# Performance work log

Hardware: AMD Instinct MI355X
Metric: run time of the kernel (lower is better)

The kernel has to match this reference:

```python
import jax, jax.numpy as jnp
import numpy as np

B, N, L = 16, 512, 2048          # batch, decoder word positions, lstm char positions
DIM, M, CE, VOCAB, H = 768, 8, 64, 1024, 128  # hidden, max_word_len, char_emb, vocab, lstm hidden


def setup_inputs() -> dict:
    key = jax.random.key(0)
    ks = jax.random.split(key, 10)
    return {
        "dec_hidden": jax.random.normal(ks[0], (B, N, DIM), jnp.float32),
        "lstm_input_ids": jax.random.randint(ks[1], (B, L), 0, VOCAB),
        "lstm_word_lens": jax.random.randint(ks[2], (B, N), 0, M + 1),
        "char_emb": jax.random.normal(ks[3], (VOCAB, CE), jnp.float32) * 0.02,
        "W_proj": jax.random.normal(ks[4], (DIM, CE * M), jnp.float32) * 0.02,
        "b_proj": jnp.zeros((CE * M,), jnp.float32),
        "W_ih": jax.random.normal(ks[5], (4 * H, 2 * CE), jnp.float32) * 0.05,
        "W_hh": jax.random.normal(ks[6], (4 * H, H), jnp.float32) * 0.05,
        "b_ih": jnp.zeros((4 * H,), jnp.float32),
        "b_hh": jnp.zeros((4 * H,), jnp.float32),
        "W_pred": jax.random.normal(ks[7], (H, VOCAB), jnp.float32) * 0.02,
        "b_pred": jnp.zeros((VOCAB,), jnp.float32),
    }


def _gather_pad(rep, lens):
    """Ragged select + left-compact + zero-pad for one batch element.
    rep: [N, M, CE] per-word char projections; lens: [N] word lengths in [0, M].
    Equivalent to: rep[mask] (ragged), truncated to L, written into zeros[L, CE]."""
    mask = jnp.arange(M) < lens[:, None]                 # [N, M]
    mflat = mask.reshape(-1)                             # [N*M]
    dest = jnp.cumsum(mflat) - 1                         # compacted destination index
    # invalid or overflowing entries are dumped into a scratch row L (dropped)
    dest = jnp.where(mflat & (dest < L), dest, L)
    vals = rep.reshape(-1, CE) * mflat[:, None].astype(rep.dtype)
    buf = jnp.zeros((L + 1, CE), rep.dtype).at[dest].set(vals)
    return buf[:L]


def _lstm(x, W_ih, W_hh, b_ih, b_hh):
    """PyTorch-convention single-layer LSTM. x: [B, T, in]. Gates order i,f,g,o."""
    def step(carry, xt):
        h, c = carry
        g = xt @ W_ih.T + b_ih + h @ W_hh.T + b_hh       # [B, 4H]
        i, f, gg, o = jnp.split(g, 4, axis=-1)
        c = jax.nn.sigmoid(f) * c + jax.nn.sigmoid(i) * jnp.tanh(gg)
        h = jax.nn.sigmoid(o) * jnp.tanh(c)
        return (h, c), h
    h0 = jnp.zeros((x.shape[0], H), x.dtype)
    _, hs = jax.lax.scan(step, (h0, h0), jnp.swapaxes(x, 0, 1))
    return jnp.swapaxes(hs, 0, 1)                        # [B, T, H]


def reference(dec_hidden, lstm_input_ids, lstm_word_lens, char_emb, W_proj, b_proj,
              W_ih, W_hh, b_ih, b_hh, W_pred, b_pred):
    dec_char = char_emb[lstm_input_ids]                  # [B, L, CE]
    # hidden_proj: b n (m d) -> b n m d
    rep = (dec_hidden @ W_proj + b_proj).reshape(B, N, M, CE)
    padded = jax.vmap(_gather_pad)(rep, lstm_word_lens)  # [B, L, CE]
    x = jnp.concatenate([dec_char, padded], axis=-1)     # [B, L, 2*CE]
    hs = _lstm(x, W_ih, W_hh, b_ih, b_hh)                # [B, L, H]
    return hs @ W_pred + b_pred                          # [B, L, VOCAB]
```

## Files before the change

### kernel.cpp

```cpp
#include <hip/hip_runtime.h>
#include <cstdint>
#include <cstddef>

#define B_    16
#define N_    512
#define L_    2048
#define DIM_  768
#define M_    8
#define CE_   64
#define VOCAB_ 1024
#define H_    128
#define G4_   512
#define XDIM_ 128

typedef __bf16 bf16x8 __attribute__((ext_vector_type(8)));
typedef float  f32x4  __attribute__((ext_vector_type(4)));

__device__ __forceinline__ unsigned short f2bf(float f) {
    unsigned u = __float_as_uint(f);
    u += 0x7fffu + ((u >> 16) & 1u);
    return (unsigned short)(u >> 16);
}

template<bool TRANSB>
__global__ __launch_bounds__(256) void gemm_f32(
    const float* __restrict__ A, const float* __restrict__ Bm,
    const float* __restrict__ bias1, const float* __restrict__ bias2,
    float* __restrict__ C, int M, int N, int K)
{
    __shared__ float As[2][8][128];
    __shared__ float Bs[2][8][128];
    const int t  = threadIdx.x;
    const int tx = t & 15, ty = t >> 4;
    const int m0 = blockIdx.y * 128, n0 = blockIdx.x * 128;
    const int arow = t >> 1, ahalf = (t & 1) * 4;
    const int bk = t >> 5, bn = (t & 31) * 4;

    float acc[8][8];
#pragma unroll
    for (int i = 0; i < 8; i++)
#pragma unroll
        for (int j = 0; j < 8; j++) acc[i][j] = 0.f;

    {
        float4 av = *(const float4*)(A + (size_t)(m0 + arow) * K + ahalf);
        float4 bv;
        if (TRANSB) bv = *(const float4*)(Bm + (size_t)(n0 + arow) * K + ahalf);
        else        bv = *(const float4*)(Bm + (size_t)bk * N + n0 + bn);
        As[0][ahalf + 0][arow] = av.x;
        As[0][ahalf + 1][arow] = av.y;
        As[0][ahalf + 2][arow] = av.z;
        As[0][ahalf + 3][arow] = av.w;
        if (TRANSB) {
            Bs[0][ahalf + 0][arow] = bv.x;
            Bs[0][ahalf + 1][arow] = bv.y;
            Bs[0][ahalf + 2][arow] = bv.z;
            Bs[0][ahalf + 3][arow] = bv.w;
        } else {
            *(float4*)&Bs[0][bk][bn] = bv;
        }
    }
    __syncthreads();

    int cur = 0;
    for (int k0 = 0; k0 < K; k0 += 8) {
        const bool more = (k0 + 8 < K);
        float4 av, bv;
        if (more) {
            av = *(const float4*)(A + (size_t)(m0 + arow) * K + (k0 + 8) + ahalf);
            if (TRANSB) bv = *(const float4*)(Bm + (size_t)(n0 + arow) * K + (k0 + 8) + ahalf);
            else        bv = *(const float4*)(Bm + (size_t)(k0 + 8 + bk) * N + n0 + bn);
        }
#pragma unroll
        for (int k = 0; k < 8; k++) {
            float a[8], bb[8];
            *(float4*)&a[0]  = *(const float4*)&As[cur][k][ty * 8];
            *(float4*)&a[4]  = *(const float4*)&As[cur][k][ty * 8 + 4];
            *(float4*)&bb[0] = *(const float4*)&Bs[cur][k][tx * 8];
            *(float4*)&bb[4] = *(const float4*)&Bs[cur][k][tx * 8 + 4];
#pragma unroll
            for (int i = 0; i < 8; i++)
#pragma unroll
                for (int j = 0; j < 8; j++)
                    acc[i][j] = fmaf(a[i], bb[j], acc[i][j]);
        }
        if (more) {
            const int nxt = cur ^ 1;
            As[nxt][ahalf + 0][arow] = av.x;
            As[nxt][ahalf + 1][arow] = av.y;
            As[nxt][ahalf + 2][arow] = av.z;
            As[nxt][ahalf + 3][arow] = av.w;
            if (TRANSB) {
                Bs[nxt][ahalf + 0][arow] = bv.x;
                Bs[nxt][ahalf + 1][arow] = bv.y;
                Bs[nxt][ahalf + 2][arow] = bv.z;
                Bs[nxt][ahalf + 3][arow] = bv.w;
            } else {
                *(float4*)&Bs[nxt][bk][bn] = bv;
            }
        }
        __syncthreads();
        cur ^= 1;
    }

    float bia[8];
#pragma unroll
    for (int j = 0; j < 8; j++) {
        int gn = n0 + tx * 8 + j;
        bia[j] = bias1[gn] + (bias2 ? bias2[gn] : 0.f);
    }
#pragma unroll
    for (int i = 0; i < 8; i++) {
        size_t row = (size_t)(m0 + ty * 8 + i) * N + n0 + tx * 8;
#pragma unroll
        for (int j = 0; j < 8; j++)
            C[row + j] = acc[i][j] + bia[j];
    }
}

__global__ __launch_bounds__(512) void scan_lens(const int* __restrict__ lens,
                                                 int* __restrict__ off)
{
    const int b = blockIdx.x, t = threadIdx.x;
    __shared__ int s[512];
    int v = lens[b * N_ + t];
    s[t] = v;
    __syncthreads();
    for (int d = 1; d < 512; d <<= 1) {
        int u = (t >= d) ? s[t - d] : 0;
        __syncthreads();
        s[t] += u;
        __syncthreads();
    }
    off[b * N_ + t] = s[t] - v;
}

__global__ __launch_bounds__(256) void char_gather(const int* __restrict__ ids,
                                                   const float* __restrict__ emb,
                                                   float* __restrict__ x)
{
    int g   = blockIdx.x * 8 + (threadIdx.x >> 5);
    int l32 = threadIdx.x & 31;
    int id  = ids[g];
    float4 v;
    if (l32 < 16) v = *(const float4*)(emb + (size_t)id * CE_ + l32 * 4);
    else          v = make_float4(0.f, 0.f, 0.f, 0.f);
    *(float4*)(x + (size_t)g * XDIM_ + l32 * 4) = v;
}

__global__ __launch_bounds__(512) void scatter_pad(const float* __restrict__ rep,
                                                   const int* __restrict__ lens,
                                                   const int* __restrict__ off,
                                                   float* __restrict__ x)
{
    int word = blockIdx.x;
    int b = word >> 9;
    int m  = threadIdx.x >> 6;
    int cc = threadIdx.x & 63;
    int len = lens[word];
    if (m < len) {
        int dst = off[word] + m;
        if (dst < L_) {
            x[((size_t)b * L_ + dst) * XDIM_ + CE_ + cc] =
                rep[((size_t)word * M_ + m) * CE_ + cc];
        }
    }
}

__global__ __launch_bounds__(512) void lstm_rec(const float* __restrict__ gx,
                                                const float* __restrict__ Whh,
                                                float* __restrict__ hs)
{
    const int b    = blockIdx.x;
    const int tid  = threadIdx.x;
    const int wave = tid >> 6, lane = tid & 63;
    const int quad = lane >> 4, l15 = lane & 15;
    const int j    = wave * 16 + l15;

    __shared__ __align__(16) unsigned short hbuf[2][128];
    if (tid < 128) hbuf[0][tid] = 0;

    bf16x8 bfrag[4][4];
#pragma unroll
    for (int q = 0; q < 4; q++) {
        const float* wrow = Whh + (size_t)(q * 128 + j) * H_;
#pragma unroll
        for (int kk = 0; kk < 4; kk++) {
            int kb = kk * 32 + quad * 8;
            float4 w0 = *(const float4*)(wrow + kb);
            float4 w1 = *(const float4*)(wrow + kb + 4);
            union { unsigned short u[8]; bf16x8 v; } U;
            U.u[0] = f2bf(w0.x); U.u[1] = f2bf(w0.y); U.u[2] = f2bf(w0.z); U.u[3] = f2bf(w0.w);
            U.u[4] = f2bf(w1.x); U.u[5] = f2bf(w1.y); U.u[6] = f2bf(w1.z); U.u[7] = f2bf(w1.w);
            bfrag[q][kk] = U.v;
        }
    }

    const float* gxb = gx + (size_t)b * L_ * G4_ + j;
    float pf[4][4];
#pragma unroll
    for (int u = 0; u < 4; u++)
#pragma unroll
        for (int q = 0; q < 4; q++)
            pf[u][q] = gxb[(size_t)u * G4_ + q * 128];

    float c = 0.f;
    float* hsb = hs + (size_t)b * L_ * H_;
    __syncthreads();

#define RCP_(x) __builtin_amdgcn_rcpf(x)
#define MFMA_(a, bb, cc) __builtin_amdgcn_mfma_f32_16x16x32_bf16(a, bb, cc, 0, 0, 0)

    for (int t0 = 0; t0 < L_; t0 += 4) {
#pragma unroll
        for (int u = 0; u < 4; u++) {
            const int t  = t0 + u;
            const int pb = t & 1;

            bf16x8 a0 = *(const bf16x8*)&hbuf[pb][0 * 32 + quad * 8];
            bf16x8 a1 = *(const bf16x8*)&hbuf[pb][1 * 32 + quad * 8];
            bf16x8 a2 = *(const bf16x8*)&hbuf[pb][2 * 32 + quad * 8];
            bf16x8 a3 = *(const bf16x8*)&hbuf[pb][3 * 32 + quad * 8];

            f32x4 accga = {pf[u][2], 0.f, 0.f, 0.f};
            f32x4 accgb = {0.f, 0.f, 0.f, 0.f};
            f32x4 acci  = {pf[u][0], 0.f, 0.f, 0.f};
            f32x4 accf  = {pf[u][1], 0.f, 0.f, 0.f};
            f32x4 acco  = {pf[u][3], 0.f, 0.f, 0.f};

            {
                int tn = t + 4; if (tn > L_ - 1) tn = L_ - 1;
#pragma unroll
                for (int q = 0; q < 4; q++) pf[u][q] = gxb[(size_t)tn * G4_ + q * 128];
            }

            accga = MFMA_(a0, bfrag[2][0], accga);
            accgb = MFMA_(a1, bfrag[2][1], accgb);
            acci  = MFMA_(a0, bfrag[0][0], acci);
            accf  = MFMA_(a0, bfrag[1][0], accf);
            acco  = MFMA_(a0, bfrag[3][0], acco);
            accga = MFMA_(a2, bfrag[2][2], accga);
            accgb = MFMA_(a3, bfrag[2][3], accgb);
            acci  = MFMA_(a1, bfrag[0][1], acci);
            accf  = MFMA_(a1, bfrag[1][1], accf);
            acco  = MFMA_(a1, bfrag[3][1], acco);
            acci  = MFMA_(a2, bfrag[0][2], acci);
            accf  = MFMA_(a2, bfrag[1][2], accf);
            acco  = MFMA_(a2, bfrag[3][2], acco);
            acci  = MFMA_(a3, bfrag[0][3], acci);
            accf  = MFMA_(a3, bfrag[1][3], accf);
            acco  = MFMA_(a3, bfrag[3][3], acco);

            float gg = accga[0] + accgb[0];
            float tg = 1.f - 2.f * RCP_(__expf(2.f * gg) + 1.f);
            float si = RCP_(1.f + __expf(-acci[0]));
            float sf = RCP_(1.f + __expf(-accf[0]));
            float so = RCP_(1.f + __expf(-acco[0]));
            c = sf * c + si * tg;
            float tc = 1.f - 2.f * RCP_(__expf(2.f * c) + 1.f);
            float h = so * tc;

            unsigned hr;
            asm("v_cvt_pk_bf16_f32 %0, %1, %2" : "=v"(hr) : "v"(h), "v"(h));
            if (quad == 0) {
                hbuf[pb ^ 1][j] = (unsigned short)hr;
                hsb[(size_t)t * H_ + j] = h;
            }
            asm volatile("s_waitcnt lgkmcnt(0)\n\ts_barrier" ::: "memory");
        }
    }
#undef RCP_
#undef MFMA_
}

extern "C" void kernel_launch(void* const* d_in, const int* in_sizes, int n_in,
                              void* d_out, int out_size, void* d_ws, size_t ws_size,
                              hipStream_t stream)
{
    (void)in_sizes; (void)n_in; (void)out_size; (void)ws_size;
    const float* dec_hidden = (const float*)d_in[0];
    const int*   ids        = (const int*)d_in[1];
    const int*   lens       = (const int*)d_in[2];
    const float* char_emb   = (const float*)d_in[3];
    const float* W_proj     = (const float*)d_in[4];
    const float* b_proj     = (const float*)d_in[5];
    const float* W_ih       = (const float*)d_in[6];
    const float* W_hh       = (const float*)d_in[7];
    const float* b_ih       = (const float*)d_in[8];
    const float* b_hh       = (const float*)d_in[9];
    const float* W_pred     = (const float*)d_in[10];
    const float* b_pred     = (const float*)d_in[11];
    float* out = (float*)d_out;

    char* ws   = (char*)d_ws;
    float* rep = (float*)(ws);
    float* x   = (float*)(ws + (size_t)16 * 1024 * 1024);
    float* hs  = (float*)(ws + (size_t)32 * 1024 * 1024);
    int*   off = (int*)  (ws + (size_t)48 * 1024 * 1024);
    float* gx  = out;

    gemm_f32<false><<<dim3(4, 64), 256, 0, stream>>>(
        dec_hidden, W_proj, b_proj, nullptr, rep, B_ * N_, 512, DIM_);

    scan_lens<<<B_, 512, 0, stream>>>(lens, off);

    char_gather<<<(B_ * L_) / 8, 256, 0, stream>>>(ids, char_emb, x);
    scatter_pad<<<B_ * N_, 512, 0, stream>>>(rep, lens, off, x);

    gemm_f32<true><<<dim3(4, 256), 256, 0, stream>>>(
        x, W_ih, b_ih, b_hh, gx, B_ * L_, G4_, XDIM_);

    lstm_rec<<<B_, 512, 0, stream>>>(gx, W_hh, hs);

    gemm_f32<false><<<dim3(8, 256), 256, 0, stream>>>(
        hs, W_pred, b_pred, nullptr, out, B_ * L_, VOCAB_, H_);
}
```

Measured before the change: 1.366 ms.

## Halve LSTM recurrence block to 4 waves, each computing two hidden-unit groups

```diff
diff --git a/kernel.cpp b/kernel.cpp
--- a/kernel.cpp
+++ b/kernel.cpp
@@ -167,53 +167,64 @@
     }
 }
 
-__global__ __launch_bounds__(512) void lstm_rec(const float* __restrict__ gx,
-                                                const float* __restrict__ Whh,
-                                                float* __restrict__ hs)
+__global__ __launch_bounds__(256, 1) void lstm_rec(const float* __restrict__ gx,
+                                                   const float* __restrict__ Whh,
+                                                   float* __restrict__ hs)
 {
     const int b    = blockIdx.x;
     const int tid  = threadIdx.x;
     const int wave = tid >> 6, lane = tid & 63;
     const int quad = lane >> 4, l15 = lane & 15;
-    const int j    = wave * 16 + l15;
+    const int jA   = wave * 32 + l15;
 
     __shared__ __align__(16) unsigned short hbuf[2][128];
     if (tid < 128) hbuf[0][tid] = 0;
 
-    bf16x8 bfrag[4][4];
-#pragma unroll
-    for (int q = 0; q < 4; q++) {
-        const float* wrow = Whh + (size_t)(q * 128 + j) * H_;
-#pragma unroll
-        for (int kk = 0; kk < 4; kk++) {
-            int kb = kk * 32 + quad * 8;
-            float4 w0 = *(const float4*)(wrow + kb);
-            float4 w1 = *(const float4*)(wrow + kb + 4);
-            union { unsigned short u[8]; bf16x8 v; } U;
-            U.u[0] = f2bf(w0.x); U.u[1] = f2bf(w0.y); U.u[2] = f2bf(w0.z); U.u[3] = f2bf(w0.w);
-            U.u[4] = f2bf(w1.x); U.u[5] = f2bf(w1.y); U.u[6] = f2bf(w1.z); U.u[7] = f2bf(w1.w);
-            bfrag[q][kk] = U.v;
-        }
-    }
-
-    const float* gxb = gx + (size_t)b * L_ * G4_ + j;
-    float pf[4][4];
-#pragma unroll
-    for (int u = 0; u < 4; u++)
-#pragma unroll
-        for (int q = 0; q < 4; q++)
-            pf[u][q] = gxb[(size_t)u * G4_ + q * 128];
+    bf16x8 bfrag[2][4][4];
+#pragma unroll
+    for (int jg = 0; jg < 2; jg++)
+#pragma unroll
+        for (int q = 0; q < 4; q++) {
+            const float* wrow = Whh + (size_t)(q * 128 + jA + jg * 16) * H_;
+#pragma unroll
+            for (int kk = 0; kk < 4; kk++) {
+                int kb = kk * 32 + quad * 8;
+                float4 w0 = *(const float4*)(wrow + kb);
+                float4 w1 = *(const float4*)(wrow + kb + 4);
+                union { unsigned short u[8]; bf16x8 v; } U;
+                U.u[0] = f2bf(w0.x); U.u[1] = f2bf(w0.y); U.u[2] = f2bf(w0.z); U.u[3] = f2bf(w0.w);
+                U.u[4] = f2bf(w1.x); U.u[5] = f2bf(w1.y); U.u[6] = f2bf(w1.z); U.u[7] = f2bf(w1.w);
+                bfrag[jg][q][kk] = U.v;
+            }
+        }
+
+    const float* gp = gx + (size_t)b * L_ * G4_ + jA;
+    float pf[2][2][4];
+#pragma unroll
+    for (int u = 0; u < 2; u++)
+#pragma unroll
+        for (int jg = 0; jg < 2; jg++)
+#pragma unroll
+            for (int q = 0; q < 4; q++)
+                pf[u][jg][q] = gp[(size_t)u * G4_ + q * 128 + jg * 16];
+    gp += 2 * G4_;
+
+    f32x4 aAi = {0,0,0,0}, aAf = aAi, aAg = aAi, aAo = aAi;
+    f32x4 aBi = aAi, aBf = aAi, aBg = aAi, aBo = aAi;
 
     float c = 0.f;
     float* hsb = hs + (size_t)b * L_ * H_;
+    const bool hi = (quad & 1);
+    const int  jw = jA + (quad & 1) * 16;
+
     __syncthreads();
 
 #define RCP_(x) __builtin_amdgcn_rcpf(x)
 #define MFMA_(a, bb, cc) __builtin_amdgcn_mfma_f32_16x16x32_bf16(a, bb, cc, 0, 0, 0)
 
-    for (int t0 = 0; t0 < L_; t0 += 4) {
-#pragma unroll
-        for (int u = 0; u < 4; u++) {
+    for (int t0 = 0; t0 < L_; t0 += 2) {
+#pragma unroll
+        for (int u = 0; u < 2; u++) {
             const int t  = t0 + u;
             const int pb = t & 1;
 
@@ -222,49 +233,72 @@
             bf16x8 a2 = *(const bf16x8*)&hbuf[pb][2 * 32 + quad * 8];
             bf16x8 a3 = *(const bf16x8*)&hbuf[pb][3 * 32 + quad * 8];
 
-            f32x4 accga = {pf[u][2], 0.f, 0.f, 0.f};
-            f32x4 accgb = {0.f, 0.f, 0.f, 0.f};
-            f32x4 acci  = {pf[u][0], 0.f, 0.f, 0.f};
-            f32x4 accf  = {pf[u][1], 0.f, 0.f, 0.f};
-            f32x4 acco  = {pf[u][3], 0.f, 0.f, 0.f};
-
-            {
-                int tn = t + 4; if (tn > L_ - 1) tn = L_ - 1;
-#pragma unroll
-                for (int q = 0; q < 4; q++) pf[u][q] = gxb[(size_t)tn * G4_ + q * 128];
-            }
-
-            accga = MFMA_(a0, bfrag[2][0], accga);
-            accgb = MFMA_(a1, bfrag[2][1], accgb);
-            acci  = MFMA_(a0, bfrag[0][0], acci);
-            accf  = MFMA_(a0, bfrag[1][0], accf);
-            acco  = MFMA_(a0, bfrag[3][0], acco);
-            accga = MFMA_(a2, bfrag[2][2], accga);
-            accgb = MFMA_(a3, bfrag[2][3], accgb);
-            acci  = MFMA_(a1, bfrag[0][1], acci);
-            accf  = MFMA_(a1, bfrag[1][1], accf);
-            acco  = MFMA_(a1, bfrag[3][1], acco);
-            acci  = MFMA_(a2, bfrag[0][2], acci);
-            accf  = MFMA_(a2, bfrag[1][2], accf);
-            acco  = MFMA_(a2, bfrag[3][2], acco);
-            acci  = MFMA_(a3, bfrag[0][3], acci);
-            accf  = MFMA_(a3, bfrag[1][3], accf);
-            acco  = MFMA_(a3, bfrag[3][3], acco);
-
-            float gg = accga[0] + accgb[0];
+            aAi[0] = pf[u][0][0]; aAf[0] = pf[u][0][1];
+            aAg[0] = pf[u][0][2]; aAo[0] = pf[u][0][3];
+            aBi[0] = pf[u][1][0]; aBf[0] = pf[u][1][1];
+            aBg[0] = pf[u][1][2]; aBo[0] = pf[u][1][3];
+
+#pragma unroll
+            for (int jg = 0; jg < 2; jg++)
+#pragma unroll
+                for (int q = 0; q < 4; q++)
+                    pf[u][jg][q] = gp[q * 128 + jg * 16];
+            gp += G4_;
+
+            aAg = MFMA_(a0, bfrag[0][2][0], aAg);
+            aBg = MFMA_(a0, bfrag[1][2][0], aBg);
+            aAi = MFMA_(a0, bfrag[0][0][0], aAi);
+            aBi = MFMA_(a0, bfrag[1][0][0], aBi);
+            aAf = MFMA_(a0, bfrag[0][1][0], aAf);
+            aBf = MFMA_(a0, bfrag[1][1][0], aBf);
+            aAo = MFMA_(a0, bfrag[0][3][0], aAo);
+            aBo = MFMA_(a0, bfrag[1][3][0], aBo);
+
+            aAg = MFMA_(a1, bfrag[0][2][1], aAg);
+            aBg = MFMA_(a1, bfrag[1][2][1], aBg);
+            aAi = MFMA_(a1, bfrag[0][0][1], aAi);
+            aBi = MFMA_(a1, bfrag[1][0][1], aBi);
+            aAf = MFMA_(a1, bfrag[0][1][1], aAf);
+            aBf = MFMA_(a1, bfrag[1][1][1], aBf);
+            aAo = MFMA_(a1, bfrag[0][3][1], aAo);
+            aBo = MFMA_(a1, bfrag[1][3][1], aBo);
+
+            aAg = MFMA_(a2, bfrag[0][2][2], aAg);
+            aBg = MFMA_(a2, bfrag[1][2][2], aBg);
+            aAi = MFMA_(a2, bfrag[0][0][2], aAi);
+            aBi = MFMA_(a2, bfrag[1][0][2], aBi);
+            aAf = MFMA_(a2, bfrag[0][1][2], aAf);
+            aBf = MFMA_(a2, bfrag[1][1][2], aBf);
+            aAo = MFMA_(a2, bfrag[0][3][2], aAo);
+            aBo = MFMA_(a2, bfrag[1][3][2], aBo);
+
+            aAg = MFMA_(a3, bfrag[0][2][3], aAg);
+            aBg = MFMA_(a3, bfrag[1][2][3], aBg);
+            aAi = MFMA_(a3, bfrag[0][0][3], aAi);
+            aBi = MFMA_(a3, bfrag[1][0][3], aBi);
+            aAf = MFMA_(a3, bfrag[0][1][3], aAf);
+            aBf = MFMA_(a3, bfrag[1][1][3], aBf);
+            aAo = MFMA_(a3, bfrag[0][3][3], aAo);
+            aBo = MFMA_(a3, bfrag[1][3][3], aBo);
+
+            float gi = hi ? aBi[0] : aAi[0];
+            float gf = hi ? aBf[0] : aAf[0];
+            float gg = hi ? aBg[0] : aAg[0];
+            float go = hi ? aBo[0] : aAo[0];
+
             float tg = 1.f - 2.f * RCP_(__expf(2.f * gg) + 1.f);
-            float si = RCP_(1.f + __expf(-acci[0]));
-            float sf = RCP_(1.f + __expf(-accf[0]));
-            float so = RCP_(1.f + __expf(-acco[0]));
+            float si = RCP_(1.f + __expf(-gi));
+            float sf = RCP_(1.f + __expf(-gf));
+            float so = RCP_(1.f + __expf(-go));
             c = sf * c + si * tg;
             float tc = 1.f - 2.f * RCP_(__expf(2.f * c) + 1.f);
             float h = so * tc;
 
             unsigned hr;
             asm("v_cvt_pk_bf16_f32 %0, %1, %2" : "=v"(hr) : "v"(h), "v"(h));
-            if (quad == 0) {
-                hbuf[pb ^ 1][j] = (unsigned short)hr;
-                hsb[(size_t)t * H_ + j] = h;
+            if (quad < 2) {
+                hbuf[pb ^ 1][jw] = (unsigned short)hr;
+                hsb[(size_t)t * H_ + jw] = h;
             }
             asm volatile("s_waitcnt lgkmcnt(0)\n\ts_barrier" ::: "memory");
         }
@@ -310,7 +344,7 @@
     gemm_f32<true><<<dim3(4, 256), 256, 0, stream>>>(
         x, W_ih, b_ih, b_hh, gx, B_ * L_, G4_, XDIM_);
 
-    lstm_rec<<<B_, 512, 0, stream>>>(gx, W_hh, hs);
+    lstm_rec<<<B_, 256, 0, stream>>>(gx, W_hh, hs);
 
     gemm_f32<false><<<dim3(8, 256), 256, 0, stream>>>(
         hs, W_pred, b_pred, nullptr, out, B_ * L_, VOCAB_, H_);
```

Result: slower. 1.436 ms (+5.1%).

## Interleave two batch sequences per LSTM block to overlap MFMA and activation latency

Applied to the files above, without the earlier changes.

```diff
diff --git a/kernel.cpp b/kernel.cpp
--- a/kernel.cpp
+++ b/kernel.cpp
@@ -167,18 +167,18 @@
     }
 }
 
-__global__ __launch_bounds__(512) void lstm_rec(const float* __restrict__ gx,
-                                                const float* __restrict__ Whh,
-                                                float* __restrict__ hs)
-{
-    const int b    = blockIdx.x;
+__global__ __launch_bounds__(512, 2) void lstm_rec(const float* __restrict__ gx,
+                                                   const float* __restrict__ Whh,
+                                                   float* __restrict__ hs)
+{
+    const int blk  = blockIdx.x;
     const int tid  = threadIdx.x;
     const int wave = tid >> 6, lane = tid & 63;
     const int quad = lane >> 4, l15 = lane & 15;
     const int j    = wave * 16 + l15;
 
-    __shared__ __align__(16) unsigned short hbuf[2][128];
-    if (tid < 128) hbuf[0][tid] = 0;
+    __shared__ __align__(16) unsigned short hbuf[2][2][128];
+    if (tid < 128) { hbuf[0][0][tid] = 0; hbuf[1][0][tid] = 0; }
 
     bf16x8 bfrag[4][4];
 #pragma unroll
@@ -196,79 +196,112 @@
         }
     }
 
-    const float* gxb = gx + (size_t)b * L_ * G4_ + j;
-    float pf[4][4];
-#pragma unroll
-    for (int u = 0; u < 4; u++)
-#pragma unroll
-        for (int q = 0; q < 4; q++)
-            pf[u][q] = gxb[(size_t)u * G4_ + q * 128];
-
-    float c = 0.f;
-    float* hsb = hs + (size_t)b * L_ * H_;
+    const float scale = (quad == 2) ? 2.f : 1.f;
+    const float postm = (quad == 2) ? 2.f : 1.f;
+    const float posta = (quad == 2) ? -1.f : 0.f;
+    const int ad0 = (0 * 16 + l15) * 4;
+    const int ad1 = (1 * 16 + l15) * 4;
+    const int ad2 = (2 * 16 + l15) * 4;
+    const int ad3 = (3 * 16 + l15) * 4;
+
+    const float* gp2[2] = { gx + (size_t)(blk * 2 + 0) * L_ * G4_ + j,
+                            gx + (size_t)(blk * 2 + 1) * L_ * G4_ + j };
+    float pf[2][4][4];
+#pragma unroll
+    for (int bb = 0; bb < 2; bb++) {
+#pragma unroll
+        for (int u = 0; u < 4; u++)
+#pragma unroll
+            for (int q = 0; q < 4; q++)
+                pf[bb][u][q] = gp2[bb][(size_t)u * G4_ + q * 128];
+        gp2[bb] += 4 * G4_;
+    }
+
+    f32x4 acc[2][4];
+#pragma unroll
+    for (int bb = 0; bb < 2; bb++) {
+#pragma unroll
+        for (int q = 0; q < 4; q++) {
+            acc[bb][q] = f32x4{pf[bb][0][q], 0.f, 0.f, 0.f};
+            pf[bb][0][q] = gp2[bb][q * 128];
+        }
+        gp2[bb] += G4_;
+    }
+
+    float  c2[2]  = {0.f, 0.f};
+    float* hp2[2] = { hs + (size_t)(blk * 2 + 0) * L_ * H_ + j,
+                      hs + (size_t)(blk * 2 + 1) * L_ * H_ + j };
+
     __syncthreads();
 
 #define RCP_(x) __builtin_amdgcn_rcpf(x)
 #define MFMA_(a, bb, cc) __builtin_amdgcn_mfma_f32_16x16x32_bf16(a, bb, cc, 0, 0, 0)
+#define INTERVAL(MB, AB, RP, WP, SLOT)                                        \
+    {                                                                         \
+        bf16x8 a0 = *(const bf16x8*)&hbuf[MB][RP][ 0 + quad * 8];             \
+        bf16x8 a1 = *(const bf16x8*)&hbuf[MB][RP][32 + quad * 8];             \
+        bf16x8 a2 = *(const bf16x8*)&hbuf[MB][RP][64 + quad * 8];             \
+        bf16x8 a3 = *(const bf16x8*)&hbuf[MB][RP][96 + quad * 8];             \
+        acc[MB][0] = MFMA_(a0, bfrag[0][0], acc[MB][0]);                      \
+        acc[MB][1] = MFMA_(a0, bfrag[1][0], acc[MB][1]);                      \
+        acc[MB][2] = MFMA_(a0, bfrag[2][0], acc[MB][2]);                      \
+        acc[MB][3] = MFMA_(a0, bfrag[3][0], acc[MB][3]);                      \
+        acc[MB][0] = MFMA_(a1, bfrag[0][1], acc[MB][0]);                      \
+        acc[MB][1] = MFMA_(a1, bfrag[1][1], acc[MB][1]);                      \
+        acc[MB][2] = MFMA_(a1, bfrag[2][1], acc[MB][2]);                      \
+        acc[MB][3] = MFMA_(a1, bfrag[3][1], acc[MB][3]);                      \
+        acc[MB][0] = MFMA_(a2, bfrag[0][2], acc[MB][0]);                      \
+        acc[MB][1] = MFMA_(a2, bfrag[1][2], acc[MB][1]);                      \
+        acc[MB][2] = MFMA_(a2, bfrag[2][2], acc[MB][2]);                      \
+        acc[MB][3] = MFMA_(a2, bfrag[3][2], acc[MB][3]);                      \
+        acc[MB][0] = MFMA_(a3, bfrag[0][3], acc[MB][0]);                      \
+        acc[MB][1] = MFMA_(a3, bfrag[1][3], acc[MB][1]);                      \
+        acc[MB][2] = MFMA_(a3, bfrag[2][3], acc[MB][2]);                      \
+        acc[MB][3] = MFMA_(a3, bfrag[3][3], acc[MB][3]);                      \
+                       \
+        float own = (quad == 0) ? acc[AB][0][0]                               \
+                  : (quad == 1) ? acc[AB][1][0]                               \
+                  : (quad == 2) ? acc[AB][2][0] : acc[AB][3][0];              \
+        float val = RCP_(1.f + __expf(-scale * own));                         \
+        float res = fmaf(val, postm, posta);                                  \
+        int ri = __float_as_int(res);                                         \
+        float si = __int_as_float(__builtin_amdgcn_ds_bpermute(ad0, ri));     \
+        float sf = __int_as_float(__builtin_amdgcn_ds_bpermute(ad1, ri));     \
+        float tg = __int_as_float(__builtin_amdgcn_ds_bpermute(ad2, ri));     \
+        float so = __int_as_float(__builtin_amdgcn_ds_bpermute(ad3, ri));     \
+        c2[AB] = sf * c2[AB] + si * tg;                                       \
+        float tcv = fmaf(RCP_(1.f + __expf(-2.f * c2[AB])), 2.f, -1.f);       \
+        float h = so * tcv;                                                   \
+        unsigned hr;                                                          \
+        asm("v_cvt_pk_bf16_f32 %0, %1, %2" : "=v"(hr) : "v"(h), "v"(h));      \
+        if (quad == 0) {                                                      \
+            hbuf[AB][WP][j] = (unsigned short)hr;                             \
+            *hp2[AB] = h;                                                     \
+        }                                                                     \
+        hp2[AB] += H_;                                                        \
+        acc[AB][0][0] = pf[AB][SLOT][0];                                      \
+        acc[AB][1][0] = pf[AB][SLOT][1];                                      \
+        acc[AB][2][0] = pf[AB][SLOT][2];                                      \
+        acc[AB][3][0] = pf[AB][SLOT][3];                                      \
+        pf[AB][SLOT][0] = gp2[AB][0];                                         \
+        pf[AB][SLOT][1] = gp2[AB][128];                                       \
+        pf[AB][SLOT][2] = gp2[AB][256];                                       \
+        pf[AB][SLOT][3] = gp2[AB][384];                                       \
+        gp2[AB] += G4_;                                                       \
+        asm volatile("s_waitcnt lgkmcnt(0)\n\ts_barrier" ::: "memory");       \
+    }
 
     for (int t0 = 0; t0 < L_; t0 += 4) {
-#pragma unroll
-        for (int u = 0; u < 4; u++) {
-            const int t  = t0 + u;
-            const int pb = t & 1;
-
-            bf16x8 a0 = *(const bf16x8*)&hbuf[pb][0 * 32 + quad * 8];
-            bf16x8 a1 = *(const bf16x8*)&hbuf[pb][1 * 32 + quad * 8];
-            bf16x8 a2 = *(const bf16x8*)&hbuf[pb][2 * 32 + quad * 8];
-            bf16x8 a3 = *(const bf16x8*)&hbuf[pb][3 * 32 + quad * 8];
-
-            f32x4 accga = {pf[u][2], 0.f, 0.f, 0.f};
-            f32x4 accgb = {0.f, 0.f, 0.f, 0.f};
-            f32x4 acci  = {pf[u][0], 0.f, 0.f, 0.f};
-            f32x4 accf  = {pf[u][1], 0.f, 0.f, 0.f};
-            f32x4 acco  = {pf[u][3], 0.f, 0.f, 0.f};
-
-            {
-                int tn = t + 4; if (tn > L_ - 1) tn = L_ - 1;
-#pragma unroll
-                for (int q = 0; q < 4; q++) pf[u][q] = gxb[(size_t)tn * G4_ + q * 128];
-            }
-
-            accga = MFMA_(a0, bfrag[2][0], accga);
-            accgb = MFMA_(a1, bfrag[2][1], accgb);
-            acci  = MFMA_(a0, bfrag[0][0], acci);
-            accf  = MFMA_(a0, bfrag[1][0], accf);
-            acco  = MFMA_(a0, bfrag[3][0], acco);
-            accga = MFMA_(a2, bfrag[2][2], accga);
-            accgb = MFMA_(a3, bfrag[2][3], accgb);
-            acci  = MFMA_(a1, bfrag[0][1], acci);
-            accf  = MFMA_(a1, bfrag[1][1], accf);
-            acco  = MFMA_(a1, bfrag[3][1], acco);
-            acci  = MFMA_(a2, bfrag[0][2], acci);
-            accf  = MFMA_(a2, bfrag[1][2], accf);
-            acco  = MFMA_(a2, bfrag[3][2], acco);
-            acci  = MFMA_(a3, bfrag[0][3], acci);
-            accf  = MFMA_(a3, bfrag[1][3], accf);
-            acco  = MFMA_(a3, bfrag[3][3], acco);
-
-            float gg = accga[0] + accgb[0];
-            float tg = 1.f - 2.f * RCP_(__expf(2.f * gg) + 1.f);
-            float si = RCP_(1.f + __expf(-acci[0]));
-            float sf = RCP_(1.f + __expf(-accf[0]));
-            float so = RCP_(1.f + __expf(-acco[0]));
-            c = sf * c + si * tg;
-            float tc = 1.f - 2.f * RCP_(__expf(2.f * c) + 1.f);
-            float h = so * tc;
-
-            unsigned hr;
-            asm("v_cvt_pk_bf16_f32 %0, %1, %2" : "=v"(hr) : "v"(h), "v"(h));
-            if (quad == 0) {
-                hbuf[pb ^ 1][j] = (unsigned short)hr;
-                hsb[(size_t)t * H_ + j] = h;
-            }
-            asm volatile("s_waitcnt lgkmcnt(0)\n\ts_barrier" ::: "memory");
-        }
-    }
+        INTERVAL(0, 1, 0, 1, 1)
+        INTERVAL(1, 0, 1, 1, 1)
+        INTERVAL(0, 1, 1, 0, 2)
+        INTERVAL(1, 0, 0, 0, 2)
+        INTERVAL(0, 1, 0, 1, 3)
+        INTERVAL(1, 0, 1, 1, 3)
+        INTERVAL(0, 1, 1, 0, 0)
+        INTERVAL(1, 0, 0, 0, 0)
+    }
+#undef INTERVAL
 #undef RCP_
 #undef MFMA_
 }
@@ -310,7 +343,7 @@
     gemm_f32<true><<<dim3(4, 256), 256, 0, stream>>>(
         x, W_ih, b_ih, b_hh, gx, B_ * L_, G4_, XDIM_);
 
-    lstm_rec<<<B_, 512, 0, stream>>>(gx, W_hh, hs);
+    lstm_rec<<<B_ / 2, 512, 0, stream>>>(gx, W_hh, hs);
 
     gemm_f32<false><<<dim3(8, 256), 256, 0, stream>>>(
         hs, W_pred, b_pred, nullptr, out, B_ * L_, VOCAB_, H_);
```

Result: slower. 2.512 ms (+83.9%).
